# Performance work log

Hardware: AMD Instinct MI355X
Metric: run time of the kernel (lower is better)

## Reference

```python
import jax, jax.numpy as jnp
import numpy as np

B, T, E, H, C = 128, 1024, 256, 256, 2


def setup_inputs() -> dict:
    key = jax.random.key(0)
    ks = jax.random.split(key, 10)
    s = 1.0 / np.sqrt(H)  # torch LSTMCell / Linear init scale
    u = lambda k, shape: jax.random.uniform(k, shape, jnp.float32, -s, s)
    return {
        "embeddings": jax.random.normal(ks[0], (B, T, E), jnp.float32),
        "mask": jnp.ones((B, T), jnp.float32),
        # forward-direction LSTMCell params (gate order i, f, g, o like torch)
        "W_ih_f": u(ks[1], (4 * H, E)),
        "W_hh_f": u(ks[2], (4 * H, H)),
        "b_f": u(ks[3], (4 * H,)),  # = b_ih + b_hh fused (mathematically identical)
        # backward-direction LSTMCell params
        "W_ih_b": u(ks[4], (4 * H, E)),
        "W_hh_b": u(ks[5], (4 * H, H)),
        "b_b": u(ks[6], (4 * H,)),
        # linear head
        "W_lin": u(ks[7], (C, 2 * H)),
        "b_lin": u(ks[8], (C,)),
    }


def _lstm_meanpool(x, W_ih, W_hh, b):
    """Run an LSTMCell recurrence over time and return mean of hidden states.
    x: [B, T, E] -> returns [B, H]."""
    Bsz, Tlen = x.shape[0], x.shape[1]
    Hdim = W_hh.shape[1]
    # precompute input contribution for all steps: [T, B, 4H]
    xg = jnp.swapaxes(jnp.einsum('bte,ge->btg', x, W_ih) + b, 0, 1)

    def step(carry, g_t):
        h, c = carry
        gates = g_t + h @ W_hh.T
        i, f, g, o = jnp.split(gates, 4, axis=-1)
        c = jax.nn.sigmoid(f) * c + jax.nn.sigmoid(i) * jnp.tanh(g)
        h = jax.nn.sigmoid(o) * jnp.tanh(c)
        return (h, c), h

    h0 = jnp.zeros((Bsz, Hdim), x.dtype)
    _, hs = jax.lax.scan(step, (h0, h0), xg)  # hs: [T, B, H]
    return hs.sum(axis=0) / float(Tlen)


def reference(embeddings, mask, W_ih_f, W_hh_f, b_f, W_ih_b, W_hh_b, b_b, W_lin, b_lin):
    x = embeddings * mask[..., None]            # mask padded positions
    h_f = _lstm_meanpool(x, W_ih_f, W_hh_f, b_f)            # forward direction
    h_b = _lstm_meanpool(x[:, ::-1], W_ih_b, W_hh_b, b_b)   # backward direction
    states = jnp.concatenate([h_f, h_b], axis=-1)           # [B, 2H]
    return states @ W_lin.T + b_lin                         # [B, C]
```

## Files before the change

kernel.cpp:

```cpp
#include <hip/hip_runtime.h>


#define B_ 128
#define T_ 1024
#define E_ 256
#define H_ 256

typedef short short8 __attribute__((ext_vector_type(8)));
typedef float f32x4 __attribute__((ext_vector_type(4)));
typedef float f32x2 __attribute__((ext_vector_type(2)));

__device__ __forceinline__ unsigned short f2bf(float f) {
  unsigned u = __builtin_bit_cast(unsigned, f);
  u += 0x7fffu + ((u >> 16) & 1u);
  return (unsigned short)(u >> 16);
}
__device__ __forceinline__ f32x4 mfma16(short8 a, short8 b, f32x4 c) {
  return __builtin_amdgcn_mfma_f32_16x16x32_bf16(a, b, c, 0, 0, 0);
}
__device__ __forceinline__ float rcpf(float x) { return __builtin_amdgcn_rcpf(x); }

__device__ __forceinline__ float lstm_ew(float gi, float gf, float gg, float go, float& c) {
  float ei = __expf(-gi), ef = __expf(-gf), eg = __expf(-2.f * gg);
  float di = 1.f + ei, df = 1.f + ef, dg = 1.f + eg;
  float r1 = rcpf(di * dg);
  float si = r1 * dg;
  float tg = 2.f * (r1 * di) - 1.f;
  c = rcpf(df) * c + si * tg;
  float eo = __expf(-go), ec = __expf(2.f * c);
  float do_ = 1.f + eo, dc = 1.f + ec;
  float r3 = rcpf(do_ * dc);
  float so = r3 * dc;
  float th = 1.f - 2.f * (r3 * do_);
  return so * th;
}

__device__ __forceinline__ short8 cvt8(f32x4 v0, f32x4 v1) {
  short8 o;
  o[0] = (short)f2bf(v0[0]); o[1] = (short)f2bf(v0[1]);
  o[2] = (short)f2bf(v0[2]); o[3] = (short)f2bf(v0[3]);
  o[4] = (short)f2bf(v1[0]); o[5] = (short)f2bf(v1[1]);
  o[6] = (short)f2bf(v1[2]); o[7] = (short)f2bf(v1[3]);
  return o;
}

__device__ __forceinline__ void bar_lds() {
  asm volatile("s_waitcnt lgkmcnt(0)" ::: "memory");
  __builtin_amdgcn_s_barrier();
}

__device__ __forceinline__ void gload16(const void* g, void* l) {
  __builtin_amdgcn_global_load_lds(
      (const __attribute__((address_space(1))) void*)g,
      (__attribute__((address_space(3))) void*)l, 16, 0, 0);
}

__global__ __launch_bounds__(256, 4) void prep_kernel(
    const float* __restrict__ x, const float* __restrict__ mask,
    unsigned short* __restrict__ img) {
  int gid = blockIdx.x * 256 + threadIdx.x;
  int i = gid & 511;
  int tt = (gid >> 9) & 1023;
  int bblk = gid >> 19;
  int r = i >> 5, s = i & 31, kc = (s - r) & 31;
  int b = bblk * 16 + r;
  const f32x4* src = (const f32x4*)(x + ((size_t)b * T_ + tt) * E_ + kc * 8);
  float mk = mask[(size_t)b * T_ + tt];
  ((short8*)img)[gid] = cvt8(src[0] * mk, src[1] * mk);
}

#define REC_STEP(PAR, TT, MORE_)                                                \
  {                                                                             \
    const bool more_ = (MORE_);                                                 \
    if constexpr (PREP) {                                                       \
      if ((TT) + 2 < T_) {                                                      \
        gload16(gsrc, (char*)XS[PAR] + w * 1024);                               \
        gsrc += dstep;                                                          \
      }                                                                         \
    }                                                                           \
    f32x4 xv0, xv1;                                                             \
    float mk = 0.f;                                                             \
    if constexpr (!PREP) {                                                      \
      if (more_) {                                                              \
        int ts = d ? (T_ - 2 - (TT)) : ((TT) + 1);                              \
        const f32x4* px = (const f32x4*)(x + ((size_t)gb_s * T_ + ts) * E_ + sc * 8); \
        xv0 = px[0]; xv1 = px[1];                                               \
        mk = mask[(size_t)gb_s * T_ + ts];                                      \
      }                                                                         \
    }                                                                           \
    {                                                                           \
      const char* hsP = (const char*)HS[PAR];                                   \
      _Pragma("unroll") for (int kp = 0; kp < 4; ++kp) {                        \
        short8 b0 = *(const short8*)(hsP + ro[2 * kp]);                         \
        short8 b1 = *(const short8*)(hsP + ro[2 * kp + 1]);                     \
        acc[0] = mfma16(wh[0][2 * kp], b0, acc[0]);                             \
        acc[1] = mfma16(wh[1][2 * kp], b0, acc[1]);                             \
        accB[0] = mfma16(wh[0][2 * kp + 1], b1, accB[0]);                       \
        accB[1] = mfma16(wh[1][2 * kp + 1], b1, accB[1]);                       \
      }                                                                         \
    }                                                                           \
    float h0 = lstm_ew(acc[0][0] + accB[0][0], acc[0][1] + accB[0][1],          \
                       acc[0][2] + accB[0][2], acc[0][3] + accB[0][3], cs[0]);  \
    float h1 = lstm_ew(acc[1][0] + accB[1][0], acc[1][1] + accB[1][1],          \
                       acc[1][2] + accB[1][2], acc[1][3] + accB[1][3], cs[1]);  \
    hsums[0] += h0;                                                             \
    hsums[1] += h1;                                                             \
    if (more_) {                                                                \
      const unsigned tag = (unsigned)((TT) + 1);                                \
      unsigned long long* __restrict__ hb = (PAR) ? Hb0 : Hb1;                  \
      unsigned pay;                                                             \
      asm("v_cvt_pk_bf16_f32 %0, %1, %2" : "=v"(pay) : "v"(h0), "v"(h1));       \
      unsigned long long wrd = (((unsigned long long)tag) << 32) | (unsigned long long)pay; \
      __hip_atomic_store(&hb[pubIdx], wrd, __ATOMIC_RELAXED,                    \
                         __HIP_MEMORY_SCOPE_AGENT);                             \
      asm volatile("" ::: "memory");                                            \
      *(int*)((char*)HS[1 - (PAR)] + ownOff) = (int)pay;                        \
      if constexpr (!PREP) {                                                    \
        ((short8*)XS[1 - (PAR)])[sr * 32 + ((sc + sr) & 31)] = cvt8(xv0 * mk, xv1 * mk); \
        bar_lds();                                                              \
      }                                                                         \
      acc[0] = bias4[0];                                                        \
      acc[1] = bias4[1];                                                        \
      accB[0] = (f32x4){0.f, 0.f, 0.f, 0.f};                                    \
      accB[1] = (f32x4){0.f, 0.f, 0.f, 0.f};                                    \
      {                                                                         \
        const char* xsP = (const char*)XS[1 - (PAR)];                           \
        _Pragma("unroll") for (int kp = 0; kp < 4; ++kp) {                      \
          short8 b0 = *(const short8*)(xsP + ro[2 * kp]);                       \
          short8 b1 = *(const short8*)(xsP + ro[2 * kp + 1]);                   \
          acc[0] = mfma16(wi[0][2 * kp], b0, acc[0]);                           \
          acc[1] = mfma16(wi[1][2 * kp], b0, acc[1]);                           \
          accB[0] = mfma16(wi[0][2 * kp + 1], b1, accB[0]);                     \
          accB[1] = mfma16(wi[1][2 * kp + 1], b1, accB[1]);                     \
        }                                                                       \
      }                                                                         \
      unsigned long long v0 = __hip_atomic_load(&hb[p0], __ATOMIC_RELAXED,      \
                                                __HIP_MEMORY_SCOPE_AGENT);      \
      unsigned long long v1 = __hip_atomic_load(&hb[p1], __ATOMIC_RELAXED,      \
                                                __HIP_MEMORY_SCOPE_AGENT);      \
      unsigned long long v2 = __hip_atomic_load(&hb[p2], __ATOMIC_RELAXED,      \
                                                __HIP_MEMORY_SCOPE_AGENT);      \
      asm volatile("" ::: "memory");                                            \
      while (((unsigned)(v0 >> 32) != tag) | ((unsigned)(v1 >> 32) != tag) |    \
             ((unsigned)(v2 >> 32) != tag)) {                                   \
        if ((unsigned)(v0 >> 32) != tag)                                        \
          v0 = __hip_atomic_load(&hb[p0], __ATOMIC_RELAXED, __HIP_MEMORY_SCOPE_AGENT); \
        if ((unsigned)(v1 >> 32) != tag)                                        \
          v1 = __hip_atomic_load(&hb[p1], __ATOMIC_RELAXED, __HIP_MEMORY_SCOPE_AGENT); \
        if ((unsigned)(v2 >> 32) != tag)                                        \
          v2 = __hip_atomic_load(&hb[p2], __ATOMIC_RELAXED, __HIP_MEMORY_SCOPE_AGENT); \
        asm volatile("" ::: "memory");                                          \
      }                                                                         \
      char* hw = (char*)HS[1 - (PAR)];                                          \
      *(int*)(hw + uo0) = (int)(unsigned)v0;                                    \
      *(int*)(hw + uo1) = (int)(unsigned)v1;                                    \
      *(int*)(hw + uo2) = (int)(unsigned)v2;                                    \
      bar_lds();                                                                \
    }                                                                           \
  }

template <bool PREP>
__global__ __launch_bounds__(512, 1) void rec_kernel(
    const float* __restrict__ x, const float* __restrict__ mask,
    const unsigned short* __restrict__ img,
    const float* __restrict__ WihF, const float* __restrict__ WhhF,
    const float* __restrict__ bF, const float* __restrict__ WihB,
    const float* __restrict__ WhhB, const float* __restrict__ bB,
    unsigned long long* __restrict__ Hbuf, float* __restrict__ hsum) {
  __shared__ __align__(16) short XS[2][16 * 256];
  __shared__ __align__(16) short HS[2][16 * 256];

  const int bid = blockIdx.x;
  const int g = bid & 15, m = bid >> 4;
  const int d = g >> 3, bblk = g & 7;
  const int tid = threadIdx.x;
  const int w = tid >> 6, l = tid & 63, l15 = l & 15, l4 = l >> 4;
  const int sr = tid >> 5, sc = tid & 31;
  const int gb_s = bblk * 16 + sr;

  const float* Wih = d ? WihB : WihF;
  const float* Whh = d ? WhhB : WhhF;
  const float* bias = d ? bB : bF;

  short8 wi[2][8], wh[2][8];
#pragma unroll
  for (int i = 0; i < 2; ++i) {
    int u_row = w * 8 + (l15 >> 2) * 2 + i;
    size_t nat = (size_t)((l15 & 3) * 256 + m * 64 + u_row);
#pragma unroll
    for (int kb = 0; kb < 8; ++kb) {
      const f32x4* pi = (const f32x4*)(Wih + nat * E_ + kb * 32 + l4 * 8);
      wi[i][kb] = cvt8(pi[0], pi[1]);
      const f32x4* ph = (const f32x4*)(Whh + nat * H_ + kb * 32 + l4 * 8);
      wh[i][kb] = cvt8(ph[0], ph[1]);
    }
  }
  f32x4 bias4[2];
#pragma unroll
  for (int i = 0; i < 2; ++i)
#pragma unroll
    for (int r = 0; r < 4; ++r)
      bias4[i][r] = bias[r * 256 + m * 64 + w * 8 + l4 * 2 + i];

  int ro[8];
#pragma unroll
  for (int kp = 0; kp < 4; ++kp) {
    ro[2 * kp] = l15 * 512 + ((((kp * 8 + l4) + l15) & 31) << 4);
    ro[2 * kp + 1] = l15 * 512 + ((((kp * 8 + 4 + l4) + l15) & 31) << 4);
  }
  const int pubIdx = (m * 32 + w * 4 + l4) * 16 + l15;
  const int ownOff = l15 * 512 + ((((m * 8 + w) + l15) & 31) << 4) + l4 * 4;
  int pp = tid * 3;
  const int p0 = pp + (pp >= m * 512 ? 512 : 0);
  const int p1 = pp + 1 + (pp + 1 >= m * 512 ? 512 : 0);
  const int p2 = pp + 2 + (pp + 2 >= m * 512 ? 512 : 0);
#define UOFF(p) (((p) & 15) * 512 + (((((p) >> 6) + ((p) & 15)) & 31) << 4) + ((((p) >> 4) & 3) * 4))
  const int uo0 = UOFF(p0), uo1 = UOFF(p1), uo2 = UOFF(p2);
#undef UOFF
  unsigned long long* __restrict__ Hb0 = Hbuf + ((size_t)g * 2 + 0) * 2048;
  unsigned long long* __restrict__ Hb1 = Hbuf + ((size_t)g * 2 + 1) * 2048;

  const int dstep = d ? -8192 : 8192;
  const char* gsrc = (const char*)img +
      ((size_t)(bblk * 1024 + (d ? (T_ - 1) : 0)) * 8192) + (size_t)tid * 16;

  ((int4*)HS)[tid] = (int4){0, 0, 0, 0};
  if constexpr (PREP) {
    gload16(gsrc, (char*)XS[0] + w * 1024);
    gload16(gsrc + dstep, (char*)XS[1] + w * 1024);
    gsrc += 2 * dstep;
  } else {
    int ts = d ? (T_ - 1) : 0;
    const f32x4* px = (const f32x4*)(x + ((size_t)gb_s * T_ + ts) * E_ + sc * 8);
    float mk = mask[(size_t)gb_s * T_ + ts];
    ((short8*)XS[0])[sr * 32 + ((sc + sr) & 31)] = cvt8(px[0] * mk, px[1] * mk);
  }
  __syncthreads();

  f32x4 acc[2], accB[2];
  acc[0] = bias4[0];
  acc[1] = bias4[1];
  accB[0] = (f32x4){0.f, 0.f, 0.f, 0.f};
  accB[1] = (f32x4){0.f, 0.f, 0.f, 0.f};
  {
    const char* xsP = (const char*)XS[0];
#pragma unroll
    for (int kp = 0; kp < 4; ++kp) {
      short8 b0 = *(const short8*)(xsP + ro[2 * kp]);
      short8 b1 = *(const short8*)(xsP + ro[2 * kp + 1]);
      acc[0] = mfma16(wi[0][2 * kp], b0, acc[0]);
      acc[1] = mfma16(wi[1][2 * kp], b0, acc[1]);
      accB[0] = mfma16(wi[0][2 * kp + 1], b1, accB[0]);
      accB[1] = mfma16(wi[1][2 * kp + 1], b1, accB[1]);
    }
  }
  __syncthreads();

  float cs[2] = {0.f, 0.f};
  float hsums[2] = {0.f, 0.f};

  for (int t2 = 0; t2 < 511; ++t2) {
    const int tt = t2 * 2;
    REC_STEP(0, tt, true);
    REC_STEP(1, tt + 1, true);
  }
  REC_STEP(0, 1022, true);
  REC_STEP(1, 1023, false);

  {
    int gb_t = bblk * 16 + l15;
    int gu = m * 64 + w * 8 + l4 * 2;
    *(f32x2*)(hsum + ((size_t)d * B_ + gb_t) * H_ + gu) = (f32x2){hsums[0], hsums[1]};
  }
}

__global__ __launch_bounds__(256, 1) void head_kernel(
    const float* __restrict__ hsum, const float* __restrict__ Wlin,
    const float* __restrict__ blin, float* __restrict__ out) {
  int tid = threadIdx.x;
  int b = tid >> 1, c = tid & 1;
  const f32x4* hf = (const f32x4*)(hsum + (size_t)b * H_);
  const f32x4* hbk = (const f32x4*)(hsum + (size_t)B_ * H_ + (size_t)b * H_);
  const f32x4* wl = (const f32x4*)(Wlin + (size_t)c * 512);
  float s = 0.f;
  for (int j = 0; j < 64; ++j) {
    f32x4 a = hf[j], ww = wl[j];
    s += a[0] * ww[0] + a[1] * ww[1] + a[2] * ww[2] + a[3] * ww[3];
  }
  for (int j = 0; j < 64; ++j) {
    f32x4 a = hbk[j], ww = wl[64 + j];
    s += a[0] * ww[0] + a[1] * ww[1] + a[2] * ww[2] + a[3] * ww[3];
  }
  out[tid] = s * (1.0f / 1024.0f) + blin[c];
}

extern "C" void kernel_launch(void* const* d_in, const int* in_sizes, int n_in,
                              void* d_out, int out_size, void* d_ws, size_t ws_size,
                              hipStream_t stream) {
  const float* emb = (const float*)d_in[0];
  const float* mask = (const float*)d_in[1];
  const float* Wih_f = (const float*)d_in[2];
  const float* Whh_f = (const float*)d_in[3];
  const float* b_f = (const float*)d_in[4];
  const float* Wih_b = (const float*)d_in[5];
  const float* Whh_b = (const float*)d_in[6];
  const float* b_b = (const float*)d_in[7];
  const float* Wlin = (const float*)d_in[8];
  const float* blin = (const float*)d_in[9];
  float* out = (float*)d_out;

  const size_t HBUF_BYTES = (size_t)16 * 2 * 2048 * 8;
  const size_t HSUM_BYTES = (size_t)2 * B_ * H_ * 4;
  const size_t IMG_BYTES = (size_t)8 * 1024 * 512 * 16;
  if (ws_size < HBUF_BYTES + HSUM_BYTES) return;
  const bool prep = ws_size >= HBUF_BYTES + HSUM_BYTES + IMG_BYTES;

  char* ws = (char*)d_ws;
  unsigned long long* Hbuf = (unsigned long long*)ws;
  float* hsum = (float*)(ws + HBUF_BYTES);
  unsigned short* img = (unsigned short*)(ws + HBUF_BYTES + HSUM_BYTES);

  (void)hipMemsetAsync(Hbuf, 0, HBUF_BYTES, stream);
  if (prep) {
    prep_kernel<<<16384, 256, 0, stream>>>(emb, mask, img);
    rec_kernel<true><<<64, 512, 0, stream>>>(emb, mask, img, Wih_f, Whh_f, b_f,
                                             Wih_b, Whh_b, b_b, Hbuf, hsum);
  } else {
    rec_kernel<false><<<64, 512, 0, stream>>>(emb, mask, img, Wih_f, Whh_f, b_f,
                                              Wih_b, Whh_b, b_b, Hbuf, hsum);
  }
  head_kernel<<<1, 256, 0, stream>>>(hsum, Wlin, blin, out);
}
```

Measured before the change: 1.537 ms.

## Halve recurrence block to 256 threads, each lane computing four hidden units

The recurrent kernel now runs 4 waves per block instead of 8, and each lane handles four hidden units instead of two. Weight register tiles double (wi/wh [4][8]), and the split accumulator pair is merged into a single chained accumulator per unit. Publishing, polling, LDS layout offsets and x staging are all re-indexed to match. This is meant to cut intra-block barrier and wave overhead per step, at the cost of higher register pressure, longer serial MFMA chains and more polling loads per lane.

```diff
diff --git a/kernel.cpp b/kernel.cpp
--- a/kernel.cpp
+++ b/kernel.cpp
@@ -75,17 +75,21 @@
     if constexpr (PREP) {                                                       \
       if ((TT) + 2 < T_) {                                                      \
         gload16(gsrc, (char*)XS[PAR] + w * 1024);                               \
+        gload16(gsrc + 4096, (char*)XS[PAR] + 4096 + w * 1024);                 \
         gsrc += dstep;                                                          \
       }                                                                         \
     }                                                                           \
-    f32x4 xv0, xv1;                                                             \
-    float mk = 0.f;                                                             \
+    f32x4 xva0, xva1, xvb0, xvb1;                                               \
+    float mkst = 0.f;                                                           \
     if constexpr (!PREP) {                                                      \
       if (more_) {                                                              \
         int ts = d ? (T_ - 2 - (TT)) : ((TT) + 1);                              \
-        const f32x4* px = (const f32x4*)(x + ((size_t)gb_s * T_ + ts) * E_ + sc * 8); \
-        xv0 = px[0]; xv1 = px[1];                                               \
-        mk = mask[(size_t)gb_s * T_ + ts];                                      \
+        const float* xr = x + ((size_t)gb_s * T_ + ts) * E_;                    \
+        xva0 = ((const f32x4*)(xr + kc0 * 8))[0];                               \
+        xva1 = ((const f32x4*)(xr + kc0 * 8))[1];                               \
+        xvb0 = ((const f32x4*)(xr + kc1 * 8))[0];                               \
+        xvb1 = ((const f32x4*)(xr + kc1 * 8))[1];                               \
+        mkst = mask[(size_t)gb_s * T_ + ts];                                    \
       }                                                                         \
     }                                                                           \
     {                                                                           \
@@ -93,74 +97,84 @@
       _Pragma("unroll") for (int kp = 0; kp < 4; ++kp) {                        \
         short8 b0 = *(const short8*)(hsP + ro[2 * kp]);                         \
         short8 b1 = *(const short8*)(hsP + ro[2 * kp + 1]);                     \
-        acc[0] = mfma16(wh[0][2 * kp], b0, acc[0]);                             \
-        acc[1] = mfma16(wh[1][2 * kp], b0, acc[1]);                             \
-        accB[0] = mfma16(wh[0][2 * kp + 1], b1, accB[0]);                       \
-        accB[1] = mfma16(wh[1][2 * kp + 1], b1, accB[1]);                       \
+        _Pragma("unroll") for (int i = 0; i < 4; ++i) {                         \
+          acc[i] = mfma16(wh[i][2 * kp], b0, acc[i]);                           \
+          acc[i] = mfma16(wh[i][2 * kp + 1], b1, acc[i]);                       \
+        }                                                                       \
       }                                                                         \
     }                                                                           \
-    float h0 = lstm_ew(acc[0][0] + accB[0][0], acc[0][1] + accB[0][1],          \
-                       acc[0][2] + accB[0][2], acc[0][3] + accB[0][3], cs[0]);  \
-    float h1 = lstm_ew(acc[1][0] + accB[1][0], acc[1][1] + accB[1][1],          \
-                       acc[1][2] + accB[1][2], acc[1][3] + accB[1][3], cs[1]);  \
-    hsums[0] += h0;                                                             \
-    hsums[1] += h1;                                                             \
+    float h0 = lstm_ew(acc[0][0], acc[0][1], acc[0][2], acc[0][3], cs[0]);      \
+    float h1 = lstm_ew(acc[1][0], acc[1][1], acc[1][2], acc[1][3], cs[1]);      \
+    float h2 = lstm_ew(acc[2][0], acc[2][1], acc[2][2], acc[2][3], cs[2]);      \
+    float h3 = lstm_ew(acc[3][0], acc[3][1], acc[3][2], acc[3][3], cs[3]);      \
+    hsums[0] += h0; hsums[1] += h1; hsums[2] += h2; hsums[3] += h3;             \
     if (more_) {                                                                \
       const unsigned tag = (unsigned)((TT) + 1);                                \
       unsigned long long* __restrict__ hb = (PAR) ? Hb0 : Hb1;                  \
-      unsigned pay;                                                             \
-      asm("v_cvt_pk_bf16_f32 %0, %1, %2" : "=v"(pay) : "v"(h0), "v"(h1));       \
-      unsigned long long wrd = (((unsigned long long)tag) << 32) | (unsigned long long)pay; \
-      __hip_atomic_store(&hb[pubIdx], wrd, __ATOMIC_RELAXED,                    \
-                         __HIP_MEMORY_SCOPE_AGENT);                             \
+      unsigned pay0, pay1;                                                      \
+      asm("v_cvt_pk_bf16_f32 %0, %1, %2" : "=v"(pay0) : "v"(h0), "v"(h1));      \
+      asm("v_cvt_pk_bf16_f32 %0, %1, %2" : "=v"(pay1) : "v"(h2), "v"(h3));      \
+      unsigned long long w0 = (((unsigned long long)tag) << 32) | (unsigned long long)pay0; \
+      unsigned long long w1 = (((unsigned long long)tag) << 32) | (unsigned long long)pay1; \
+      __hip_atomic_store(&hb[pub0], w0, __ATOMIC_RELAXED, __HIP_MEMORY_SCOPE_AGENT); \
+      __hip_atomic_store(&hb[pub1], w1, __ATOMIC_RELAXED, __HIP_MEMORY_SCOPE_AGENT); \
       asm volatile("" ::: "memory");                                            \
-      *(int*)((char*)HS[1 - (PAR)] + ownOff) = (int)pay;                        \
+      *(int2*)((char*)HS[1 - (PAR)] + ownOff) = (int2){(int)pay0, (int)pay1};   \
       if constexpr (!PREP) {                                                    \
-        ((short8*)XS[1 - (PAR)])[sr * 32 + ((sc + sr) & 31)] = cvt8(xv0 * mk, xv1 * mk); \
+        short8* xsw = (short8*)XS[1 - (PAR)];                                   \
+        xsw[st_r * 32 + ((st_s0 + st_r) & 31)] = cvt8(xva0 * mkst, xva1 * mkst); \
+        xsw[st_r * 32 + ((st_s1 + st_r) & 31)] = cvt8(xvb0 * mkst, xvb1 * mkst); \
         bar_lds();                                                              \
       }                                                                         \
-      acc[0] = bias4[0];                                                        \
-      acc[1] = bias4[1];                                                        \
-      accB[0] = (f32x4){0.f, 0.f, 0.f, 0.f};                                    \
-      accB[1] = (f32x4){0.f, 0.f, 0.f, 0.f};                                    \
+      _Pragma("unroll") for (int i = 0; i < 4; ++i) acc[i] = bias4[i];          \
       {                                                                         \
         const char* xsP = (const char*)XS[1 - (PAR)];                           \
         _Pragma("unroll") for (int kp = 0; kp < 4; ++kp) {                      \
           short8 b0 = *(const short8*)(xsP + ro[2 * kp]);                       \
           short8 b1 = *(const short8*)(xsP + ro[2 * kp + 1]);                   \
-          acc[0] = mfma16(wi[0][2 * kp], b0, acc[0]);                           \
-          acc[1] = mfma16(wi[1][2 * kp], b0, acc[1]);                           \
-          accB[0] = mfma16(wi[0][2 * kp + 1], b1, accB[0]);                     \
-          accB[1] = mfma16(wi[1][2 * kp + 1], b1, accB[1]);                     \
+          _Pragma("unroll") for (int i = 0; i < 4; ++i) {                       \
+            acc[i] = mfma16(wi[i][2 * kp], b0, acc[i]);                         \
+            acc[i] = mfma16(wi[i][2 * kp + 1], b1, acc[i]);                     \
+          }                                                                     \
         }                                                                       \
       }                                                                         \
-      unsigned long long v0 = __hip_atomic_load(&hb[p0], __ATOMIC_RELAXED,      \
-                                                __HIP_MEMORY_SCOPE_AGENT);      \
-      unsigned long long v1 = __hip_atomic_load(&hb[p1], __ATOMIC_RELAXED,      \
-                                                __HIP_MEMORY_SCOPE_AGENT);      \
-      unsigned long long v2 = __hip_atomic_load(&hb[p2], __ATOMIC_RELAXED,      \
-                                                __HIP_MEMORY_SCOPE_AGENT);      \
+      unsigned long long v0 = __hip_atomic_load(&hb[p0], __ATOMIC_RELAXED, __HIP_MEMORY_SCOPE_AGENT); \
+      unsigned long long v1 = __hip_atomic_load(&hb[p1], __ATOMIC_RELAXED, __HIP_MEMORY_SCOPE_AGENT); \
+      unsigned long long v2 = __hip_atomic_load(&hb[p2], __ATOMIC_RELAXED, __HIP_MEMORY_SCOPE_AGENT); \
+      unsigned long long v3 = __hip_atomic_load(&hb[p3], __ATOMIC_RELAXED, __HIP_MEMORY_SCOPE_AGENT); \
+      unsigned long long v4 = __hip_atomic_load(&hb[p4], __ATOMIC_RELAXED, __HIP_MEMORY_SCOPE_AGENT); \
+      unsigned long long v5 = __hip_atomic_load(&hb[p5], __ATOMIC_RELAXED, __HIP_MEMORY_SCOPE_AGENT); \
       asm volatile("" ::: "memory");                                            \
       while (((unsigned)(v0 >> 32) != tag) | ((unsigned)(v1 >> 32) != tag) |    \
-             ((unsigned)(v2 >> 32) != tag)) {                                   \
+             ((unsigned)(v2 >> 32) != tag) | ((unsigned)(v3 >> 32) != tag) |    \
+             ((unsigned)(v4 >> 32) != tag) | ((unsigned)(v5 >> 32) != tag)) {   \
         if ((unsigned)(v0 >> 32) != tag)                                        \
           v0 = __hip_atomic_load(&hb[p0], __ATOMIC_RELAXED, __HIP_MEMORY_SCOPE_AGENT); \
         if ((unsigned)(v1 >> 32) != tag)                                        \
           v1 = __hip_atomic_load(&hb[p1], __ATOMIC_RELAXED, __HIP_MEMORY_SCOPE_AGENT); \
         if ((unsigned)(v2 >> 32) != tag)                                        \
           v2 = __hip_atomic_load(&hb[p2], __ATOMIC_RELAXED, __HIP_MEMORY_SCOPE_AGENT); \
+        if ((unsigned)(v3 >> 32) != tag)                                        \
+          v3 = __hip_atomic_load(&hb[p3], __ATOMIC_RELAXED, __HIP_MEMORY_SCOPE_AGENT); \
+        if ((unsigned)(v4 >> 32) != tag)                                        \
+          v4 = __hip_atomic_load(&hb[p4], __ATOMIC_RELAXED, __HIP_MEMORY_SCOPE_AGENT); \
+        if ((unsigned)(v5 >> 32) != tag)                                        \
+          v5 = __hip_atomic_load(&hb[p5], __ATOMIC_RELAXED, __HIP_MEMORY_SCOPE_AGENT); \
         asm volatile("" ::: "memory");                                          \
       }                                                                         \
       char* hw = (char*)HS[1 - (PAR)];                                          \
       *(int*)(hw + uo0) = (int)(unsigned)v0;                                    \
       *(int*)(hw + uo1) = (int)(unsigned)v1;                                    \
       *(int*)(hw + uo2) = (int)(unsigned)v2;                                    \
+      *(int*)(hw + uo3) = (int)(unsigned)v3;                                    \
+      *(int*)(hw + uo4) = (int)(unsigned)v4;                                    \
+      *(int*)(hw + uo5) = (int)(unsigned)v5;                                    \
       bar_lds();                                                                \
     }                                                                           \
   }
 
 template <bool PREP>
-__global__ __launch_bounds__(512, 1) void rec_kernel(
+__global__ __launch_bounds__(256, 1) void rec_kernel(
     const float* __restrict__ x, const float* __restrict__ mask,
     const unsigned short* __restrict__ img,
     const float* __restrict__ WihF, const float* __restrict__ WhhF,
@@ -175,18 +189,19 @@
   const int d = g >> 3, bblk = g & 7;
   const int tid = threadIdx.x;
   const int w = tid >> 6, l = tid & 63, l15 = l & 15, l4 = l >> 4;
-  const int sr = tid >> 5, sc = tid & 31;
-  const int gb_s = bblk * 16 + sr;
+
+  const int st_r = tid >> 4, st_s0 = (tid * 2) & 31, st_s1 = st_s0 + 1;
+  const int kc0 = (st_s0 - st_r) & 31, kc1 = (st_s1 - st_r) & 31;
+  const int gb_s = bblk * 16 + st_r;
 
   const float* Wih = d ? WihB : WihF;
   const float* Whh = d ? WhhB : WhhF;
   const float* bias = d ? bB : bF;
 
-  short8 wi[2][8], wh[2][8];
-#pragma unroll
-  for (int i = 0; i < 2; ++i) {
-    int u_row = w * 8 + (l15 >> 2) * 2 + i;
-    size_t nat = (size_t)((l15 & 3) * 256 + m * 64 + u_row);
+  short8 wi[4][8], wh[4][8];
+#pragma unroll
+  for (int i = 0; i < 4; ++i) {
+    size_t nat = (size_t)((l15 & 3) * 256 + m * 64 + 16 * w + 4 * (l15 >> 2) + i);
 #pragma unroll
     for (int kb = 0; kb < 8; ++kb) {
       const f32x4* pi = (const f32x4*)(Wih + nat * E_ + kb * 32 + l4 * 8);
@@ -195,12 +210,12 @@
       wh[i][kb] = cvt8(ph[0], ph[1]);
     }
   }
-  f32x4 bias4[2];
-#pragma unroll
-  for (int i = 0; i < 2; ++i)
+  f32x4 bias4[4];
+#pragma unroll
+  for (int i = 0; i < 4; ++i)
 #pragma unroll
     for (int r = 0; r < 4; ++r)
-      bias4[i][r] = bias[r * 256 + m * 64 + w * 8 + l4 * 2 + i];
+      bias4[i][r] = bias[r * 256 + m * 64 + 16 * w + 4 * l4 + i];
 
   int ro[8];
 #pragma unroll
@@ -208,14 +223,24 @@
     ro[2 * kp] = l15 * 512 + ((((kp * 8 + l4) + l15) & 31) << 4);
     ro[2 * kp + 1] = l15 * 512 + ((((kp * 8 + 4 + l4) + l15) & 31) << 4);
   }
-  const int pubIdx = (m * 32 + w * 4 + l4) * 16 + l15;
-  const int ownOff = l15 * 512 + ((((m * 8 + w) + l15) & 31) << 4) + l4 * 4;
-  int pp = tid * 3;
+  const int pub0 = m * 512 + w * 128 + l4 * 16 + l15;
+  const int pub1 = pub0 + 64;
+  const int ownOff =
+      l15 * 512 + ((((m * 8 + 2 * w + (l4 >> 1)) + l15) & 31) << 4) + 8 * (l4 & 1);
+  const int pp = tid * 6;
   const int p0 = pp + (pp >= m * 512 ? 512 : 0);
   const int p1 = pp + 1 + (pp + 1 >= m * 512 ? 512 : 0);
   const int p2 = pp + 2 + (pp + 2 >= m * 512 ? 512 : 0);
-#define UOFF(p) (((p) & 15) * 512 + (((((p) >> 6) + ((p) & 15)) & 31) << 4) + ((((p) >> 4) & 3) * 4))
+  const int p3 = pp + 3 + (pp + 3 >= m * 512 ? 512 : 0);
+  const int p4 = pp + 4 + (pp + 4 >= m * 512 ? 512 : 0);
+  const int p5 = pp + 5 + (pp + 5 >= m * 512 ? 512 : 0);
+#define UOFF(p)                                                                  \
+  (((p) & 15) * 512 +                                                            \
+   (((((p) >> 9) * 8 + 2 * (((p) >> 7) & 3) + ((((p) >> 4) & 3) >> 1)) +         \
+     ((p) & 15)) & 31) * 16 +                                                    \
+   8 * ((((p) >> 4) & 3) & 1) + 4 * (((p) >> 6) & 1))
   const int uo0 = UOFF(p0), uo1 = UOFF(p1), uo2 = UOFF(p2);
+  const int uo3 = UOFF(p3), uo4 = UOFF(p4), uo5 = UOFF(p5);
 #undef UOFF
   unsigned long long* __restrict__ Hb0 = Hbuf + ((size_t)g * 2 + 0) * 2048;
   unsigned long long* __restrict__ Hb1 = Hbuf + ((size_t)g * 2 + 1) * 2048;
@@ -225,39 +250,46 @@
       ((size_t)(bblk * 1024 + (d ? (T_ - 1) : 0)) * 8192) + (size_t)tid * 16;
 
   ((int4*)HS)[tid] = (int4){0, 0, 0, 0};
+  ((int4*)HS)[tid + 256] = (int4){0, 0, 0, 0};
   if constexpr (PREP) {
     gload16(gsrc, (char*)XS[0] + w * 1024);
+    gload16(gsrc + 4096, (char*)XS[0] + 4096 + w * 1024);
     gload16(gsrc + dstep, (char*)XS[1] + w * 1024);
+    gload16(gsrc + dstep + 4096, (char*)XS[1] + 4096 + w * 1024);
     gsrc += 2 * dstep;
   } else {
     int ts = d ? (T_ - 1) : 0;
-    const f32x4* px = (const f32x4*)(x + ((size_t)gb_s * T_ + ts) * E_ + sc * 8);
+    const float* xr = x + ((size_t)gb_s * T_ + ts) * E_;
     float mk = mask[(size_t)gb_s * T_ + ts];
-    ((short8*)XS[0])[sr * 32 + ((sc + sr) & 31)] = cvt8(px[0] * mk, px[1] * mk);
+    f32x4 a0 = ((const f32x4*)(xr + kc0 * 8))[0] * mk;
+    f32x4 a1 = ((const f32x4*)(xr + kc0 * 8))[1] * mk;
+    f32x4 b0 = ((const f32x4*)(xr + kc1 * 8))[0] * mk;
+    f32x4 b1 = ((const f32x4*)(xr + kc1 * 8))[1] * mk;
+    ((short8*)XS[0])[st_r * 32 + ((st_s0 + st_r) & 31)] = cvt8(a0, a1);
+    ((short8*)XS[0])[st_r * 32 + ((st_s1 + st_r) & 31)] = cvt8(b0, b1);
   }
   __syncthreads();
 
-  f32x4 acc[2], accB[2];
-  acc[0] = bias4[0];
-  acc[1] = bias4[1];
-  accB[0] = (f32x4){0.f, 0.f, 0.f, 0.f};
-  accB[1] = (f32x4){0.f, 0.f, 0.f, 0.f};
+  f32x4 acc[4];
+#pragma unroll
+  for (int i = 0; i < 4; ++i) acc[i] = bias4[i];
   {
     const char* xsP = (const char*)XS[0];
 #pragma unroll
     for (int kp = 0; kp < 4; ++kp) {
       short8 b0 = *(const short8*)(xsP + ro[2 * kp]);
       short8 b1 = *(const short8*)(xsP + ro[2 * kp + 1]);
-      acc[0] = mfma16(wi[0][2 * kp], b0, acc[0]);
-      acc[1] = mfma16(wi[1][2 * kp], b0, acc[1]);
-      accB[0] = mfma16(wi[0][2 * kp + 1], b1, accB[0]);
-      accB[1] = mfma16(wi[1][2 * kp + 1], b1, accB[1]);
+#pragma unroll
+      for (int i = 0; i < 4; ++i) {
+        acc[i] = mfma16(wi[i][2 * kp], b0, acc[i]);
+        acc[i] = mfma16(wi[i][2 * kp + 1], b1, acc[i]);
+      }
     }
   }
   __syncthreads();
 
-  float cs[2] = {0.f, 0.f};
-  float hsums[2] = {0.f, 0.f};
+  float cs[4] = {0.f, 0.f, 0.f, 0.f};
+  float hsums[4] = {0.f, 0.f, 0.f, 0.f};
 
   for (int t2 = 0; t2 < 511; ++t2) {
     const int tt = t2 * 2;
@@ -269,8 +301,9 @@
 
   {
     int gb_t = bblk * 16 + l15;
-    int gu = m * 64 + w * 8 + l4 * 2;
-    *(f32x2*)(hsum + ((size_t)d * B_ + gb_t) * H_ + gu) = (f32x2){hsums[0], hsums[1]};
+    int gu = m * 64 + 16 * w + 4 * l4;
+    *(f32x4*)(hsum + ((size_t)d * B_ + gb_t) * H_ + gu) =
+        (f32x4){hsums[0], hsums[1], hsums[2], hsums[3]};
   }
 }
 
@@ -323,10 +356,10 @@
   (void)hipMemsetAsync(Hbuf, 0, HBUF_BYTES, stream);
   if (prep) {
     prep_kernel<<<16384, 256, 0, stream>>>(emb, mask, img);
-    rec_kernel<true><<<64, 512, 0, stream>>>(emb, mask, img, Wih_f, Whh_f, b_f,
+    rec_kernel<true><<<64, 256, 0, stream>>>(emb, mask, img, Wih_f, Whh_f, b_f,
                                              Wih_b, Whh_b, b_b, Hbuf, hsum);
   } else {
-    rec_kernel<false><<<64, 512, 0, stream>>>(emb, mask, img, Wih_f, Whh_f, b_f,
+    rec_kernel<false><<<64, 256, 0, stream>>>(emb, mask, img, Wih_f, Whh_f, b_f,
                                               Wih_b, Whh_b, b_b, Hbuf, hsum);
   }
   head_kernel<<<1, 256, 0, stream>>>(hsum, Wlin, blin, out);
```

Result: slower. 2.184 ms (+42.1%).

## Process two batch blocks per workgroup to interleave independent recurrences

Applied to the files above, without the earlier changes.

Each workgroup now handles two 16-row batch blocks (A and B) instead of one, halving the grid to 32 blocks. The A and B recurrence steps are interleaved so that the MFMA and elementwise work of one block overlaps the cross-workgroup publish and poll latency of the other. This aims to hide the inter-block synchronisation latency that dominates each serial time step. In exchange each workgroup does twice the work per step, uses double the LDS, and the whole problem runs on half as many CUs.

```diff
diff --git a/kernel.cpp b/kernel.cpp
--- a/kernel.cpp
+++ b/kernel.cpp
@@ -69,92 +69,135 @@
   ((short8*)img)[gid] = cvt8(src[0] * mk, src[1] * mk);
 }
 
-#define REC_STEP(PAR, TT, MORE_)                                                \
+#define HH16(HSRC, AC, AC2, WREG)                                               \
+  {                                                                             \
+    const char* hsP = (const char*)(HSRC);                                      \
+    _Pragma("unroll") for (int kp = 0; kp < 4; ++kp) {                          \
+      short8 b0 = *(const short8*)(hsP + ro[2 * kp]);                           \
+      short8 b1 = *(const short8*)(hsP + ro[2 * kp + 1]);                       \
+      AC[0] = mfma16(WREG[0][2 * kp], b0, AC[0]);                               \
+      AC[1] = mfma16(WREG[1][2 * kp], b0, AC[1]);                               \
+      AC2[0] = mfma16(WREG[0][2 * kp + 1], b1, AC2[0]);                         \
+      AC2[1] = mfma16(WREG[1][2 * kp + 1], b1, AC2[1]);                         \
+    }                                                                           \
+  }
+
+#define POLL_ISSUE(HB, V)                                                        \
+  V[0] = __hip_atomic_load(&(HB)[p0], __ATOMIC_RELAXED, __HIP_MEMORY_SCOPE_AGENT); \
+  V[1] = __hip_atomic_load(&(HB)[p1], __ATOMIC_RELAXED, __HIP_MEMORY_SCOPE_AGENT); \
+  V[2] = __hip_atomic_load(&(HB)[p2], __ATOMIC_RELAXED, __HIP_MEMORY_SCOPE_AGENT);
+
+#define POLL_RETRY(HB, V, TAG)                                                   \
+  while (((unsigned)(V[0] >> 32) != (TAG)) | ((unsigned)(V[1] >> 32) != (TAG)) | \
+         ((unsigned)(V[2] >> 32) != (TAG))) {                                    \
+    if ((unsigned)(V[0] >> 32) != (TAG))                                         \
+      V[0] = __hip_atomic_load(&(HB)[p0], __ATOMIC_RELAXED, __HIP_MEMORY_SCOPE_AGENT); \
+    if ((unsigned)(V[1] >> 32) != (TAG))                                         \
+      V[1] = __hip_atomic_load(&(HB)[p1], __ATOMIC_RELAXED, __HIP_MEMORY_SCOPE_AGENT); \
+    if ((unsigned)(V[2] >> 32) != (TAG))                                         \
+      V[2] = __hip_atomic_load(&(HB)[p2], __ATOMIC_RELAXED, __HIP_MEMORY_SCOPE_AGENT); \
+    asm volatile("" ::: "memory");                                               \
+  }
+
+#define REC2(PAR, TT, MORE_)                                                    \
   {                                                                             \
     const bool more_ = (MORE_);                                                 \
     if constexpr (PREP) {                                                       \
       if ((TT) + 2 < T_) {                                                      \
-        gload16(gsrc, (char*)XS[PAR] + w * 1024);                               \
-        gsrc += dstep;                                                          \
-      }                                                                         \
-    }                                                                           \
-    f32x4 xv0, xv1;                                                             \
-    float mk = 0.f;                                                             \
+        gload16(gsrcA, (char*)XSa[PAR] + w * 1024);                             \
+        gload16(gsrcB, (char*)XSb[PAR] + w * 1024);                             \
+        gsrcA += dstep;                                                         \
+        gsrcB += dstep;                                                         \
+      }                                                                         \
+    }                                                                           \
+    f32x4 xva0, xva1, xvb0, xvb1;                                               \
+    float mka = 0.f, mkb = 0.f;                                                 \
     if constexpr (!PREP) {                                                      \
       if (more_) {                                                              \
         int ts = d ? (T_ - 2 - (TT)) : ((TT) + 1);                              \
-        const f32x4* px = (const f32x4*)(x + ((size_t)gb_s * T_ + ts) * E_ + sc * 8); \
-        xv0 = px[0]; xv1 = px[1];                                               \
-        mk = mask[(size_t)gb_s * T_ + ts];                                      \
-      }                                                                         \
-    }                                                                           \
-    {                                                                           \
-      const char* hsP = (const char*)HS[PAR];                                   \
-      _Pragma("unroll") for (int kp = 0; kp < 4; ++kp) {                        \
-        short8 b0 = *(const short8*)(hsP + ro[2 * kp]);                         \
-        short8 b1 = *(const short8*)(hsP + ro[2 * kp + 1]);                     \
-        acc[0] = mfma16(wh[0][2 * kp], b0, acc[0]);                             \
-        acc[1] = mfma16(wh[1][2 * kp], b0, acc[1]);                             \
-        accB[0] = mfma16(wh[0][2 * kp + 1], b1, accB[0]);                       \
-        accB[1] = mfma16(wh[1][2 * kp + 1], b1, accB[1]);                       \
-      }                                                                         \
-    }                                                                           \
-    float h0 = lstm_ew(acc[0][0] + accB[0][0], acc[0][1] + accB[0][1],          \
-                       acc[0][2] + accB[0][2], acc[0][3] + accB[0][3], cs[0]);  \
-    float h1 = lstm_ew(acc[1][0] + accB[1][0], acc[1][1] + accB[1][1],          \
-                       acc[1][2] + accB[1][2], acc[1][3] + accB[1][3], cs[1]);  \
-    hsums[0] += h0;                                                             \
-    hsums[1] += h1;                                                             \
+        const float* xrA = x + ((size_t)gbA_s * T_ + ts) * E_;                  \
+        xva0 = ((const f32x4*)(xrA + kcs * 8))[0];                              \
+        xva1 = ((const f32x4*)(xrA + kcs * 8))[1];                              \
+        mka = mask[(size_t)gbA_s * T_ + ts];                                    \
+        const float* xrB = x + ((size_t)gbB_s * T_ + ts) * E_;                  \
+        xvb0 = ((const f32x4*)(xrB + kcs * 8))[0];                              \
+        xvb1 = ((const f32x4*)(xrB + kcs * 8))[1];                              \
+        mkb = mask[(size_t)gbB_s * T_ + ts];                                    \
+      }                                                                         \
+    }                                                                           \
+    const unsigned tag = (unsigned)((TT) + 1);                                  \
+    unsigned long long* __restrict__ hbA = (PAR) ? HbA0 : HbA1;                 \
+    unsigned long long* __restrict__ hbB = (PAR) ? HbB0 : HbB1;                 \
+                                       \
+    HH16(HSa[PAR], accA, accA2, wh);                                            \
+    float h0A = lstm_ew(accA[0][0] + accA2[0][0], accA[0][1] + accA2[0][1],     \
+                        accA[0][2] + accA2[0][2], accA[0][3] + accA2[0][3], csA[0]); \
+    float h1A = lstm_ew(accA[1][0] + accA2[1][0], accA[1][1] + accA2[1][1],     \
+                        accA[1][2] + accA2[1][2], accA[1][3] + accA2[1][3], csA[1]); \
+    hsA[0] += h0A;                                                              \
+    hsA[1] += h1A;                                                              \
+    unsigned payA;                                                              \
     if (more_) {                                                                \
-      const unsigned tag = (unsigned)((TT) + 1);                                \
-      unsigned long long* __restrict__ hb = (PAR) ? Hb0 : Hb1;                  \
-      unsigned pay;                                                             \
-      asm("v_cvt_pk_bf16_f32 %0, %1, %2" : "=v"(pay) : "v"(h0), "v"(h1));       \
-      unsigned long long wrd = (((unsigned long long)tag) << 32) | (unsigned long long)pay; \
-      __hip_atomic_store(&hb[pubIdx], wrd, __ATOMIC_RELAXED,                    \
+      asm("v_cvt_pk_bf16_f32 %0, %1, %2" : "=v"(payA) : "v"(h0A), "v"(h1A));    \
+      unsigned long long wrd = (((unsigned long long)tag) << 32) | (unsigned long long)payA; \
+      __hip_atomic_store(&hbA[pubIdx], wrd, __ATOMIC_RELAXED,                   \
                          __HIP_MEMORY_SCOPE_AGENT);                             \
       asm volatile("" ::: "memory");                                            \
-      *(int*)((char*)HS[1 - (PAR)] + ownOff) = (int)pay;                        \
+      *(int*)((char*)HSa[1 - (PAR)] + ownOff) = (int)payA;                      \
+    }                                                                           \
+                                       \
+    HH16(HSb[PAR], accB_, accB2, wh);                                           \
+    float h0B = lstm_ew(accB_[0][0] + accB2[0][0], accB_[0][1] + accB2[0][1],   \
+                        accB_[0][2] + accB2[0][2], accB_[0][3] + accB2[0][3], csB[0]); \
+    float h1B = lstm_ew(accB_[1][0] + accB2[1][0], accB_[1][1] + accB2[1][1],   \
+                        accB_[1][2] + accB2[1][2], accB_[1][3] + accB2[1][3], csB[1]); \
+    hsB[0] += h0B;                                                              \
+    hsB[1] += h1B;                                                              \
+    if (more_) {                                                                \
+      unsigned payB;                                                            \
+      asm("v_cvt_pk_bf16_f32 %0, %1, %2" : "=v"(payB) : "v"(h0B), "v"(h1B));    \
+      unsigned long long wrd = (((unsigned long long)tag) << 32) | (unsigned long long)payB; \
+      __hip_atomic_store(&hbB[pubIdx], wrd, __ATOMIC_RELAXED,                   \
+                         __HIP_MEMORY_SCOPE_AGENT);                             \
+      asm volatile("" ::: "memory");                                            \
+      *(int*)((char*)HSb[1 - (PAR)] + ownOff) = (int)payB;                      \
       if constexpr (!PREP) {                                                    \
-        ((short8*)XS[1 - (PAR)])[sr * 32 + ((sc + sr) & 31)] = cvt8(xv0 * mk, xv1 * mk); \
+        ((short8*)XSa[1 - (PAR)])[st_r * 32 + ((st_s + st_r) & 31)] =           \
+            cvt8(xva0 * mka, xva1 * mka);                                       \
+        ((short8*)XSb[1 - (PAR)])[st_r * 32 + ((st_s + st_r) & 31)] =           \
+            cvt8(xvb0 * mkb, xvb1 * mkb);                                       \
         bar_lds();                                                              \
       }                                                                         \
-      acc[0] = bias4[0];                                                        \
-      acc[1] = bias4[1];                                                        \
-      accB[0] = (f32x4){0.f, 0.f, 0.f, 0.f};                                    \
-      accB[1] = (f32x4){0.f, 0.f, 0.f, 0.f};                                    \
+                           \
+      accA[0] = bias4[0];                                                       \
+      accA[1] = bias4[1];                                                       \
+      accA2[0] = (f32x4){0.f, 0.f, 0.f, 0.f};                                   \
+      accA2[1] = (f32x4){0.f, 0.f, 0.f, 0.f};                                   \
+      HH16(XSa[1 - (PAR)], accA, accA2, wi);                                    \
+      accB_[0] = bias4[0];                                                      \
+      accB_[1] = bias4[1];                                                      \
+      accB2[0] = (f32x4){0.f, 0.f, 0.f, 0.f};                                   \
+      accB2[1] = (f32x4){0.f, 0.f, 0.f, 0.f};                                   \
+      HH16(XSb[1 - (PAR)], accB_, accB2, wi);                                   \
+           \
+      unsigned long long vA[3], vB[3];                                          \
+      POLL_ISSUE(hbA, vA);                                                      \
+      POLL_ISSUE(hbB, vB);                                                      \
+      asm volatile("" ::: "memory");                                            \
+      POLL_RETRY(hbA, vA, tag);                                                 \
       {                                                                         \
-        const char* xsP = (const char*)XS[1 - (PAR)];                           \
-        _Pragma("unroll") for (int kp = 0; kp < 4; ++kp) {                      \
-          short8 b0 = *(const short8*)(xsP + ro[2 * kp]);                       \
-          short8 b1 = *(const short8*)(xsP + ro[2 * kp + 1]);                   \
-          acc[0] = mfma16(wi[0][2 * kp], b0, acc[0]);                           \
-          acc[1] = mfma16(wi[1][2 * kp], b0, acc[1]);                           \
-          accB[0] = mfma16(wi[0][2 * kp + 1], b1, accB[0]);                     \
-          accB[1] = mfma16(wi[1][2 * kp + 1], b1, accB[1]);                     \
-        }                                                                       \
-      }                                                                         \
-      unsigned long long v0 = __hip_atomic_load(&hb[p0], __ATOMIC_RELAXED,      \
-                                                __HIP_MEMORY_SCOPE_AGENT);      \
-      unsigned long long v1 = __hip_atomic_load(&hb[p1], __ATOMIC_RELAXED,      \
-                                                __HIP_MEMORY_SCOPE_AGENT);      \
-      unsigned long long v2 = __hip_atomic_load(&hb[p2], __ATOMIC_RELAXED,      \
-                                                __HIP_MEMORY_SCOPE_AGENT);      \
-      asm volatile("" ::: "memory");                                            \
-      while (((unsigned)(v0 >> 32) != tag) | ((unsigned)(v1 >> 32) != tag) |    \
-             ((unsigned)(v2 >> 32) != tag)) {                                   \
-        if ((unsigned)(v0 >> 32) != tag)                                        \
-          v0 = __hip_atomic_load(&hb[p0], __ATOMIC_RELAXED, __HIP_MEMORY_SCOPE_AGENT); \
-        if ((unsigned)(v1 >> 32) != tag)                                        \
-          v1 = __hip_atomic_load(&hb[p1], __ATOMIC_RELAXED, __HIP_MEMORY_SCOPE_AGENT); \
-        if ((unsigned)(v2 >> 32) != tag)                                        \
-          v2 = __hip_atomic_load(&hb[p2], __ATOMIC_RELAXED, __HIP_MEMORY_SCOPE_AGENT); \
-        asm volatile("" ::: "memory");                                          \
-      }                                                                         \
-      char* hw = (char*)HS[1 - (PAR)];                                          \
-      *(int*)(hw + uo0) = (int)(unsigned)v0;                                    \
-      *(int*)(hw + uo1) = (int)(unsigned)v1;                                    \
-      *(int*)(hw + uo2) = (int)(unsigned)v2;                                    \
+        char* hw = (char*)HSa[1 - (PAR)];                                       \
+        *(int*)(hw + uo0) = (int)(unsigned)vA[0];                               \
+        *(int*)(hw + uo1) = (int)(unsigned)vA[1];                               \
+        *(int*)(hw + uo2) = (int)(unsigned)vA[2];                               \
+      }                                                                         \
+      POLL_RETRY(hbB, vB, tag);                                                 \
+      {                                                                         \
+        char* hw = (char*)HSb[1 - (PAR)];                                       \
+        *(int*)(hw + uo0) = (int)(unsigned)vB[0];                               \
+        *(int*)(hw + uo1) = (int)(unsigned)vB[1];                               \
+        *(int*)(hw + uo2) = (int)(unsigned)vB[2];                               \
+      }                                                                         \
       bar_lds();                                                                \
     }                                                                           \
   }
@@ -167,16 +210,20 @@
     const float* __restrict__ bF, const float* __restrict__ WihB,
     const float* __restrict__ WhhB, const float* __restrict__ bB,
     unsigned long long* __restrict__ Hbuf, float* __restrict__ hsum) {
-  __shared__ __align__(16) short XS[2][16 * 256];
-  __shared__ __align__(16) short HS[2][16 * 256];
+  __shared__ __align__(16) short XSa[2][16 * 256], XSb[2][16 * 256];
+  __shared__ __align__(16) short HSa[2][16 * 256], HSb[2][16 * 256];
 
   const int bid = blockIdx.x;
-  const int g = bid & 15, m = bid >> 4;
-  const int d = g >> 3, bblk = g & 7;
+  const int p8 = bid & 7, m = bid >> 3;
+  const int d = p8 >> 2, pair = p8 & 3;
+  const int bblkA = 2 * pair, bblkB = 2 * pair + 1;
+  const int gA = d * 8 + bblkA, gB = d * 8 + bblkB;
   const int tid = threadIdx.x;
   const int w = tid >> 6, l = tid & 63, l15 = l & 15, l4 = l >> 4;
-  const int sr = tid >> 5, sc = tid & 31;
-  const int gb_s = bblk * 16 + sr;
+
+  const int st_r = tid >> 5, st_s = tid & 31;
+  const int kcs = (st_s - st_r) & 31;
+  const int gbA_s = bblkA * 16 + st_r, gbB_s = bblkB * 16 + st_r;
 
   const float* Wih = d ? WihB : WihF;
   const float* Whh = d ? WhhB : WhhF;
@@ -217,60 +264,72 @@
 #define UOFF(p) (((p) & 15) * 512 + (((((p) >> 6) + ((p) & 15)) & 31) << 4) + ((((p) >> 4) & 3) * 4))
   const int uo0 = UOFF(p0), uo1 = UOFF(p1), uo2 = UOFF(p2);
 #undef UOFF
-  unsigned long long* __restrict__ Hb0 = Hbuf + ((size_t)g * 2 + 0) * 2048;
-  unsigned long long* __restrict__ Hb1 = Hbuf + ((size_t)g * 2 + 1) * 2048;
+  unsigned long long* __restrict__ HbA0 = Hbuf + ((size_t)gA * 2 + 0) * 2048;
+  unsigned long long* __restrict__ HbA1 = Hbuf + ((size_t)gA * 2 + 1) * 2048;
+  unsigned long long* __restrict__ HbB0 = Hbuf + ((size_t)gB * 2 + 0) * 2048;
+  unsigned long long* __restrict__ HbB1 = Hbuf + ((size_t)gB * 2 + 1) * 2048;
 
   const int dstep = d ? -8192 : 8192;
-  const char* gsrc = (const char*)img +
-      ((size_t)(bblk * 1024 + (d ? (T_ - 1) : 0)) * 8192) + (size_t)tid * 16;
-
-  ((int4*)HS)[tid] = (int4){0, 0, 0, 0};
+  const char* imgB = (const char*)img;
+  const char* gsrcA = imgB + ((size_t)(bblkA * 1024 + (d ? (T_ - 1) : 0))) * 8192 +
+                      (size_t)tid * 16;
+  const char* gsrcB = imgB + ((size_t)(bblkB * 1024 + (d ? (T_ - 1) : 0))) * 8192 +
+                      (size_t)tid * 16;
+
+  ((int4*)HSa)[tid] = (int4){0, 0, 0, 0};
+  ((int4*)HSb)[tid] = (int4){0, 0, 0, 0};
   if constexpr (PREP) {
-    gload16(gsrc, (char*)XS[0] + w * 1024);
-    gload16(gsrc + dstep, (char*)XS[1] + w * 1024);
-    gsrc += 2 * dstep;
+    gload16(gsrcA, (char*)XSa[0] + w * 1024);
+    gload16(gsrcA + dstep, (char*)XSa[1] + w * 1024);
+    gsrcA += 2 * dstep;
+    gload16(gsrcB, (char*)XSb[0] + w * 1024);
+    gload16(gsrcB + dstep, (char*)XSb[1] + w * 1024);
+    gsrcB += 2 * dstep;
   } else {
     int ts = d ? (T_ - 1) : 0;
-    const f32x4* px = (const f32x4*)(x + ((size_t)gb_s * T_ + ts) * E_ + sc * 8);
-    float mk = mask[(size_t)gb_s * T_ + ts];
-    ((short8*)XS[0])[sr * 32 + ((sc + sr) & 31)] = cvt8(px[0] * mk, px[1] * mk);
+    const float* xrA = x + ((size_t)gbA_s * T_ + ts) * E_;
+    float mka = mask[(size_t)gbA_s * T_ + ts];
+    ((short8*)XSa[0])[st_r * 32 + ((st_s + st_r) & 31)] =
+        cvt8(((const f32x4*)(xrA + kcs * 8))[0] * mka,
+             ((const f32x4*)(xrA + kcs * 8))[1] * mka);
+    const float* xrB = x + ((size_t)gbB_s * T_ + ts) * E_;
+    float mkb = mask[(size_t)gbB_s * T_ + ts];
+    ((short8*)XSb[0])[st_r * 32 + ((st_s + st_r) & 31)] =
+        cvt8(((const f32x4*)(xrB + kcs * 8))[0] * mkb,
+             ((const f32x4*)(xrB + kcs * 8))[1] * mkb);
   }
   __syncthreads();
 
-  f32x4 acc[2], accB[2];
-  acc[0] = bias4[0];
-  acc[1] = bias4[1];
-  accB[0] = (f32x4){0.f, 0.f, 0.f, 0.f};
-  accB[1] = (f32x4){0.f, 0.f, 0.f, 0.f};
-  {
-    const char* xsP = (const char*)XS[0];
-#pragma unroll
-    for (int kp = 0; kp < 4; ++kp) {
-      short8 b0 = *(const short8*)(xsP + ro[2 * kp]);
-      short8 b1 = *(const short8*)(xsP + ro[2 * kp + 1]);
-      acc[0] = mfma16(wi[0][2 * kp], b0, acc[0]);
-      acc[1] = mfma16(wi[1][2 * kp], b0, acc[1]);
-      accB[0] = mfma16(wi[0][2 * kp + 1], b1, accB[0]);
-      accB[1] = mfma16(wi[1][2 * kp + 1], b1, accB[1]);
-    }
-  }
+  f32x4 accA[2], accA2[2], accB_[2], accB2[2];
+  accA[0] = bias4[0];
+  accA[1] = bias4[1];
+  accA2[0] = (f32x4){0.f, 0.f, 0.f, 0.f};
+  accA2[1] = (f32x4){0.f, 0.f, 0.f, 0.f};
+  HH16(XSa[0], accA, accA2, wi);
+  accB_[0] = bias4[0];
+  accB_[1] = bias4[1];
+  accB2[0] = (f32x4){0.f, 0.f, 0.f, 0.f};
+  accB2[1] = (f32x4){0.f, 0.f, 0.f, 0.f};
+  HH16(XSb[0], accB_, accB2, wi);
   __syncthreads();
 
-  float cs[2] = {0.f, 0.f};
-  float hsums[2] = {0.f, 0.f};
+  float csA[2] = {0.f, 0.f}, hsA[2] = {0.f, 0.f};
+  float csB[2] = {0.f, 0.f}, hsB[2] = {0.f, 0.f};
 
   for (int t2 = 0; t2 < 511; ++t2) {
     const int tt = t2 * 2;
-    REC_STEP(0, tt, true);
-    REC_STEP(1, tt + 1, true);
-  }
-  REC_STEP(0, 1022, true);
-  REC_STEP(1, 1023, false);
+    REC2(0, tt, true);
+    REC2(1, tt + 1, true);
+  }
+  REC2(0, 1022, true);
+  REC2(1, 1023, false);
 
   {
-    int gb_t = bblk * 16 + l15;
     int gu = m * 64 + w * 8 + l4 * 2;
-    *(f32x2*)(hsum + ((size_t)d * B_ + gb_t) * H_ + gu) = (f32x2){hsums[0], hsums[1]};
+    *(f32x2*)(hsum + ((size_t)d * B_ + bblkA * 16 + l15) * H_ + gu) =
+        (f32x2){hsA[0], hsA[1]};
+    *(f32x2*)(hsum + ((size_t)d * B_ + bblkB * 16 + l15) * H_ + gu) =
+        (f32x2){hsB[0], hsB[1]};
   }
 }
 
@@ -323,10 +382,10 @@
   (void)hipMemsetAsync(Hbuf, 0, HBUF_BYTES, stream);
   if (prep) {
     prep_kernel<<<16384, 256, 0, stream>>>(emb, mask, img);
-    rec_kernel<true><<<64, 512, 0, stream>>>(emb, mask, img, Wih_f, Whh_f, b_f,
+    rec_kernel<true><<<32, 512, 0, stream>>>(emb, mask, img, Wih_f, Whh_f, b_f,
                                              Wih_b, Whh_b, b_b, Hbuf, hsum);
   } else {
-    rec_kernel<false><<<64, 512, 0, stream>>>(emb, mask, img, Wih_f, Whh_f, b_f,
+    rec_kernel<false><<<32, 512, 0, stream>>>(emb, mask, img, Wih_f, Whh_f, b_f,
                                               Wih_b, Whh_b, b_b, Hbuf, hsum);
   }
   head_kernel<<<1, 256, 0, stream>>>(hsum, Wlin, blin, out);
```

New measurement: 5.892 ms. 283% more time.
